# Optimization experiments

Hardware: AMD Instinct MI355X
Metric: run time of the kernel (lower is better)

Reference implementation:

```python
import jax, jax.numpy as jnp
import numpy as np

BASE = 7.0  # ModularPhaseNorm modulus


def _plane_rotate(x, theta):
    # Rotate the first 2*P dims of x in P independent 2D planes by learned angles theta [P].
    P = theta.shape[0]
    c, s = jnp.cos(theta), jnp.sin(theta)  # [P]
    head = x[..., : 2 * P].reshape(x.shape[:-1] + (P, 2))
    a, b = head[..., 0], head[..., 1]
    rot = jnp.stack([c * a - s * b, s * a + c * b], axis=-1)
    rot = rot.reshape(x.shape[:-1] + (2 * P,))
    return jnp.concatenate([rot, x[..., 2 * P :]], axis=-1)


def _modular_phase_norm(x, gamma, beta, base=BASE):
    # Wrap activations into [-base/2, base/2) (modular phase), then affine per-channel.
    wrapped = x - base * jnp.floor(x / base + 0.5)
    return gamma * wrapped + beta


def setup_inputs() -> dict:
    key = jax.random.key(0)
    ks = jax.random.split(key, 8)
    B, F, T, H = 8192, 4096, 9, 32
    team_paths = jax.random.normal(ks[0], (B, F, T), dtype=jnp.float32)
    W1 = jax.random.normal(ks[1], (F, H), dtype=jnp.float32) / np.sqrt(F)
    b1 = jnp.zeros((H,), dtype=jnp.float32)
    theta1 = jax.random.normal(ks[2], (2,), dtype=jnp.float32)  # num_rotation_planes=2
    gamma = jnp.ones((H,), dtype=jnp.float32)
    beta = jnp.zeros((H,), dtype=jnp.float32)
    W2 = jax.random.normal(ks[3], (H, 1), dtype=jnp.float32) / np.sqrt(H)
    b2 = jnp.zeros((1,), dtype=jnp.float32)
    theta2 = jax.random.normal(ks[4], (2,), dtype=jnp.float32)
    return {"team_paths": team_paths, "theta1": theta1, "W1": W1, "b1": b1,
            "gamma": gamma, "beta": beta, "theta2": theta2, "W2": W2, "b2": b2}


def reference(team_paths, theta1, W1, b1, gamma, beta, theta2, W2, b2):
    # Batch the per-member Python loop: [B, F, T] -> [B, T, F]
    x = jnp.transpose(team_paths, (0, 2, 1))
    # eidosTransform(feature_dim -> 32, 2 rotation planes)
    h = _plane_rotate(x, theta1)
    h = jnp.einsum("btf,fh->bth", h, W1) + b1
    # ModularPhaseNorm(32, base=7)
    h = _modular_phase_norm(h, gamma, beta)
    # eidosTransform(32 -> 1, 2 rotation planes)
    h = _plane_rotate(h, theta2)
    scores = jnp.einsum("bth,ho->bto", h, W2)[..., 0] + b2[0]  # [B, T]
    return jax.nn.softmax(scores, axis=1)
```

## Files before the change

### kernel.cpp

```cpp
#include <hip/hip_runtime.h>
#include <math.h>

typedef float f2v __attribute__((ext_vector_type(2)));
typedef float f4v __attribute__((ext_vector_type(4)));

#define NTILE 16
#define TILE_F 2304
#define BUF_F  4608
#define FT 36864

#define GL16(gp, lp) \
    __builtin_amdgcn_global_load_lds((const __attribute__((address_space(1))) void*)(gp), \
                                     (__attribute__((address_space(3))) void*)(lp), 16, 0, 0)
#define GL4(gp, lp) \
    __builtin_amdgcn_global_load_lds((const __attribute__((address_space(1))) void*)(gp), \
                                     (__attribute__((address_space(3))) void*)(lp), 4, 0, 0)

__global__ __launch_bounds__(256) void scorer_kernel(
    const float* __restrict__ x,
    const float* __restrict__ th1,
    const float* __restrict__ W1,
    const float* __restrict__ b1,
    const float* __restrict__ gamma,
    const float* __restrict__ beta,
    const float* __restrict__ th2,
    const float* __restrict__ W2,
    const float* __restrict__ b2p,
    float* __restrict__ out)
{
    __shared__ __align__(16) float xl[2 * BUF_F];
    const int tid = threadIdx.x;
    const int wv  = tid >> 6;
    const int hg  = tid & 7;
    const int fc  = tid >> 3;
    const int b0  = blockIdx.x * 2;
    const float* xb = x + (size_t)b0 * FT;

    f2v acc[2][9][2];
    #pragma unroll
    for (int b = 0; b < 2; ++b)
        #pragma unroll
        for (int t = 0; t < 9; ++t) {
            acc[b][t][0] = (f2v){0.f, 0.f};
            acc[b][t][1] = (f2v){0.f, 0.f};
        }

    #define STAGE(tileidx, lbuf)                                            \
        do {                                                                \
            const float* gt0 = xb + (size_t)(tileidx) * TILE_F;             \
            const float* gt1 = gt0 + FT;                                    \
            float* lb = (lbuf);                                             \
            GL16(gt0 + tid * 4,        lb + wv * 256);                      \
            GL16(gt0 + 1024 + tid * 4, lb + 1024 + wv * 256);               \
            GL4 (gt0 + 2048 + tid,     lb + 2048 + wv * 64);                \
            GL16(gt1 + tid * 4,        lb + TILE_F + wv * 256);             \
            GL16(gt1 + 1024 + tid * 4, lb + TILE_F + 1024 + wv * 256);      \
            GL4 (gt1 + 2048 + tid,     lb + TILE_F + 2048 + wv * 64);       \
        } while (0)

    STAGE(0, xl);

    int cur = 0;
    for (int tile = 0; tile < NTILE; ++tile) {
        __syncthreads();
        if (tile + 1 < NTILE)
            STAGE(tile + 1, &xl[(cur ^ 1) * BUF_F]);
        if (tile == 0) {
            if (tid < 36) {
                int bb = tid / 18, r = tid % 18, t = r >> 1, p = r & 1;
                float c = cosf(th1[p]), sn = sinf(th1[p]);
                float a  = xl[bb * TILE_F + (2 * p) * 9 + t];
                float bv = xl[bb * TILE_F + (2 * p + 1) * 9 + t];
                xl[bb * TILE_F + (2 * p) * 9 + t]     = c * a - sn * bv;
                xl[bb * TILE_F + (2 * p + 1) * 9 + t] = sn * a + c * bv;
            }
            __syncthreads();
        }
        const float* xbuf = &xl[cur * BUF_F];
        const size_t fb = (size_t)tile * 256;
        #pragma unroll
        for (int i = 0; i < 8; ++i) {
            const int row = i * 32 + fc;
            f4v wq = ((const f4v*)W1)[(fb + row) * 8 + hg];
            f2v wlo = {wq.x, wq.y}, whi = {wq.z, wq.w};
            const float* xp0 = &xbuf[row * 9];
            const float* xp1 = xp0 + TILE_F;
            #pragma unroll
            for (int t = 0; t < 9; ++t) {
                f2v x0 = {xp0[t], xp0[t]};
                f2v x1 = {xp1[t], xp1[t]};
                acc[0][t][0] += x0 * wlo;
                acc[0][t][1] += x0 * whi;
                acc[1][t][0] += x1 * wlo;
                acc[1][t][1] += x1 * whi;
            }
        }
        cur ^= 1;
    }

    const int lane = tid & 63;
    float* red = xl;
    float* redbase = &red[(wv * 8 + lane) * 72];
    #pragma unroll
    for (int b = 0; b < 2; ++b)
        #pragma unroll
        for (int t = 0; t < 9; ++t)
            #pragma unroll
            for (int jv = 0; jv < 2; ++jv) {
                f2v v = acc[b][t][jv];
                v.x += __shfl_xor(v.x, 8);  v.y += __shfl_xor(v.y, 8);
                v.x += __shfl_xor(v.x, 16); v.y += __shfl_xor(v.y, 16);
                v.x += __shfl_xor(v.x, 32); v.y += __shfl_xor(v.y, 32);
                if (lane < 8) {
                    int idx = b * 36 + t * 4 + jv * 2;
                    redbase[idx]     = v.x;
                    redbase[idx + 1] = v.y;
                }
            }
    __syncthreads();

    for (int o = tid; o < 576; o += 256) {
        int h = o & 31;
        int t = (o >> 5) % 9;
        int bb = o / 288;
        int hg2 = h >> 2, j = h & 3;
        int idx = bb * 36 + t * 4 + j;
        float v = red[(0 * 8 + hg2) * 72 + idx]
                + red[(1 * 8 + hg2) * 72 + idx]
                + red[(2 * 8 + hg2) * 72 + idx]
                + red[(3 * 8 + hg2) * 72 + idx];
        v += b1[h];
        float wr = v - 7.0f * floorf(v / 7.0f + 0.5f);
        xl[2304 + bb * 288 + t * 32 + h] = gamma[h] * wr + beta[h];
    }
    __syncthreads();

    if (tid < 18) {
        int bb = tid / 9, t = tid % 9;
        const float* g = &xl[2304 + bb * 288 + t * 32];
        float c0 = cosf(th2[0]), s0 = sinf(th2[0]);
        float c1 = cosf(th2[1]), s1 = sinf(th2[1]);
        float sc = (c0 * g[0] - s0 * g[1]) * W2[0]
                 + (s0 * g[0] + c0 * g[1]) * W2[1]
                 + (c1 * g[2] - s1 * g[3]) * W2[2]
                 + (s1 * g[2] + c1 * g[3]) * W2[3];
        #pragma unroll
        for (int h = 4; h < 32; ++h) sc += g[h] * W2[h];
        sc += b2p[0];
        xl[2880 + bb * 9 + t] = sc;
    }
    __syncthreads();

    if (tid < 18) {
        int bb = tid / 9, t = tid % 9;
        const float* sb = &xl[2880 + bb * 9];
        float m = sb[0];
        #pragma unroll
        for (int k = 1; k < 9; ++k) m = fmaxf(m, sb[k]);
        float den = 0.f;
        #pragma unroll
        for (int k = 0; k < 9; ++k) den += expf(sb[k] - m);
        out[(size_t)(b0 + bb) * 9 + t] = expf(sb[t] - m) / den;
    }
}

extern "C" void kernel_launch(void* const* d_in, const int* in_sizes, int n_in,
                              void* d_out, int out_size, void* d_ws, size_t ws_size,
                              hipStream_t stream) {
    const float* x     = (const float*)d_in[0];
    const float* th1   = (const float*)d_in[1];
    const float* W1    = (const float*)d_in[2];
    const float* b1    = (const float*)d_in[3];
    const float* gamma = (const float*)d_in[4];
    const float* beta  = (const float*)d_in[5];
    const float* th2   = (const float*)d_in[6];
    const float* W2    = (const float*)d_in[7];
    const float* b2    = (const float*)d_in[8];
    float* out = (float*)d_out;

    const int B = in_sizes[0] / FT;
    dim3 grid(B / 2), block(256);
    hipLaunchKernelGGL(scorer_kernel, grid, block, 0, stream,
                       x, th1, W1, b1, gamma, beta, th2, W2, b2, out);
}
```

Before: 439.9 us.

## Process one batch row per block with register-staged transposed LDS tiles

Each block now handles a single batch element instead of two, which doubles the grid. Tiles are prefetched with nontemporal global loads into registers and scattered into LDS in a transposed [t][f] layout, replacing the direct global-to-LDS async copies. The transposed layout lets the inner loop read x with vectorized LDS loads, and W1 rows are reassigned so each thread owns 8 consecutive features. The cost is that the W1 reuse across two batch rows is lost, so W1 traffic doubles. The scattered LDS stores may also cause bank conflicts.

```diff
diff --git a/kernel.cpp b/kernel.cpp
--- a/kernel.cpp
+++ b/kernel.cpp
@@ -5,16 +5,8 @@
 typedef float f4v __attribute__((ext_vector_type(4)));
 
 #define NTILE 16
-#define TILE_F 2304
-#define BUF_F  4608
+#define TILE_W 2304
 #define FT 36864
-
-#define GL16(gp, lp) \
-    __builtin_amdgcn_global_load_lds((const __attribute__((address_space(1))) void*)(gp), \
-                                     (__attribute__((address_space(3))) void*)(lp), 16, 0, 0)
-#define GL4(gp, lp) \
-    __builtin_amdgcn_global_load_lds((const __attribute__((address_space(1))) void*)(gp), \
-                                     (__attribute__((address_space(3))) void*)(lp), 4, 0, 0)
 
 __global__ __launch_bounds__(256) void scorer_kernel(
     const float* __restrict__ x,
@@ -28,116 +20,122 @@
     const float* __restrict__ b2p,
     float* __restrict__ out)
 {
-    __shared__ __align__(16) float xl[2 * BUF_F];
+    __shared__ __align__(16) float xl[2 * TILE_W];
     const int tid = threadIdx.x;
-    const int wv  = tid >> 6;
     const int hg  = tid & 7;
     const int fc  = tid >> 3;
-    const int b0  = blockIdx.x * 2;
-    const float* xb = x + (size_t)b0 * FT;
+    const int wv  = tid >> 6;
+    const float* xb = x + (size_t)blockIdx.x * FT;
 
-    f2v acc[2][9][2];
+    f2v acc[9][2];
     #pragma unroll
-    for (int b = 0; b < 2; ++b)
-        #pragma unroll
-        for (int t = 0; t < 9; ++t) {
-            acc[b][t][0] = (f2v){0.f, 0.f};
-            acc[b][t][1] = (f2v){0.f, 0.f};
-        }
+    for (int t = 0; t < 9; ++t) {
+        acc[t][0] = (f2v){0.f, 0.f};
+        acc[t][1] = (f2v){0.f, 0.f};
+    }
 
-    #define STAGE(tileidx, lbuf)                                            \
-        do {                                                                \
-            const float* gt0 = xb + (size_t)(tileidx) * TILE_F;             \
-            const float* gt1 = gt0 + FT;                                    \
-            float* lb = (lbuf);                                             \
-            GL16(gt0 + tid * 4,        lb + wv * 256);                      \
-            GL16(gt0 + 1024 + tid * 4, lb + 1024 + wv * 256);               \
-            GL4 (gt0 + 2048 + tid,     lb + 2048 + wv * 64);                \
-            GL16(gt1 + tid * 4,        lb + TILE_F + wv * 256);             \
-            GL16(gt1 + 1024 + tid * 4, lb + TILE_F + 1024 + wv * 256);      \
-            GL4 (gt1 + 2048 + tid,     lb + TILE_F + 2048 + wv * 64);       \
-        } while (0)
+    int laddr[9];
+    #pragma unroll
+    for (int j = 0; j < 9; ++j) {
+        int w = (j < 4) ? tid * 4 + j
+              : (j < 8) ? 1024 + tid * 4 + (j - 4)
+                        : 2048 + tid;
+        int f = (unsigned)w / 9u;
+        int t = w - 9 * f;
+        laddr[j] = t * 256 + f;
+    }
 
-    STAGE(0, xl);
+    f4v s04 = __builtin_nontemporal_load((const f4v*)(xb + tid * 4));
+    f4v s47 = __builtin_nontemporal_load((const f4v*)(xb + 1024 + tid * 4));
+    float s8 = __builtin_nontemporal_load(xb + 2048 + tid);
 
+    const f4v* __restrict__ W1v = (const f4v*)W1;
     int cur = 0;
     for (int tile = 0; tile < NTILE; ++tile) {
         __syncthreads();
-        if (tile + 1 < NTILE)
-            STAGE(tile + 1, &xl[(cur ^ 1) * BUF_F]);
+        float* lb = &xl[cur * TILE_W];
+        lb[laddr[0]] = s04.x; lb[laddr[1]] = s04.y;
+        lb[laddr[2]] = s04.z; lb[laddr[3]] = s04.w;
+        lb[laddr[4]] = s47.x; lb[laddr[5]] = s47.y;
+        lb[laddr[6]] = s47.z; lb[laddr[7]] = s47.w;
+        lb[laddr[8]] = s8;
+        __syncthreads();
+        if (tile + 1 < NTILE) {
+            const float* gt = xb + (size_t)(tile + 1) * TILE_W;
+            s04 = __builtin_nontemporal_load((const f4v*)(gt + tid * 4));
+            s47 = __builtin_nontemporal_load((const f4v*)(gt + 1024 + tid * 4));
+            s8  = __builtin_nontemporal_load(gt + 2048 + tid);
+        }
         if (tile == 0) {
-            if (tid < 36) {
-                int bb = tid / 18, r = tid % 18, t = r >> 1, p = r & 1;
+            if (tid < 18) {
+                int p = tid / 9, t = tid - p * 9;
                 float c = cosf(th1[p]), sn = sinf(th1[p]);
-                float a  = xl[bb * TILE_F + (2 * p) * 9 + t];
-                float bv = xl[bb * TILE_F + (2 * p + 1) * 9 + t];
-                xl[bb * TILE_F + (2 * p) * 9 + t]     = c * a - sn * bv;
-                xl[bb * TILE_F + (2 * p + 1) * 9 + t] = sn * a + c * bv;
+                float a  = xl[t * 256 + 2 * p];
+                float bv = xl[t * 256 + 2 * p + 1];
+                xl[t * 256 + 2 * p]     = c * a - sn * bv;
+                xl[t * 256 + 2 * p + 1] = sn * a + c * bv;
             }
             __syncthreads();
         }
-        const float* xbuf = &xl[cur * BUF_F];
-        const size_t fb = (size_t)tile * 256;
+        const int fb = tile * 256;
+        f2v wlo[8], whi[8];
         #pragma unroll
         for (int i = 0; i < 8; ++i) {
-            const int row = i * 32 + fc;
-            f4v wq = ((const f4v*)W1)[(fb + row) * 8 + hg];
-            f2v wlo = {wq.x, wq.y}, whi = {wq.z, wq.w};
-            const float* xp0 = &xbuf[row * 9];
-            const float* xp1 = xp0 + TILE_F;
-            #pragma unroll
-            for (int t = 0; t < 9; ++t) {
-                f2v x0 = {xp0[t], xp0[t]};
-                f2v x1 = {xp1[t], xp1[t]};
-                acc[0][t][0] += x0 * wlo;
-                acc[0][t][1] += x0 * whi;
-                acc[1][t][0] += x1 * wlo;
-                acc[1][t][1] += x1 * whi;
-            }
+            f4v wq = W1v[(size_t)(fb + fc * 8 + i) * 8 + hg];
+            wlo[i] = (f2v){wq.x, wq.y};
+            whi[i] = (f2v){wq.z, wq.w};
+        }
+        const float* xr = &xl[cur * TILE_W + fc * 8];
+        #pragma unroll
+        for (int t = 0; t < 9; ++t) {
+            f4v xa = *(const f4v*)(xr + t * 256);
+            f4v xc = *(const f4v*)(xr + t * 256 + 4);
+            acc[t][0] += (f2v){xa.x, xa.x} * wlo[0]; acc[t][1] += (f2v){xa.x, xa.x} * whi[0];
+            acc[t][0] += (f2v){xa.y, xa.y} * wlo[1]; acc[t][1] += (f2v){xa.y, xa.y} * whi[1];
+            acc[t][0] += (f2v){xa.z, xa.z} * wlo[2]; acc[t][1] += (f2v){xa.z, xa.z} * whi[2];
+            acc[t][0] += (f2v){xa.w, xa.w} * wlo[3]; acc[t][1] += (f2v){xa.w, xa.w} * whi[3];
+            acc[t][0] += (f2v){xc.x, xc.x} * wlo[4]; acc[t][1] += (f2v){xc.x, xc.x} * whi[4];
+            acc[t][0] += (f2v){xc.y, xc.y} * wlo[5]; acc[t][1] += (f2v){xc.y, xc.y} * whi[5];
+            acc[t][0] += (f2v){xc.z, xc.z} * wlo[6]; acc[t][1] += (f2v){xc.z, xc.z} * whi[6];
+            acc[t][0] += (f2v){xc.w, xc.w} * wlo[7]; acc[t][1] += (f2v){xc.w, xc.w} * whi[7];
         }
         cur ^= 1;
     }
 
     const int lane = tid & 63;
     float* red = xl;
-    float* redbase = &red[(wv * 8 + lane) * 72];
+    float* redbase = &red[(wv * 8 + lane) * 36];
     #pragma unroll
-    for (int b = 0; b < 2; ++b)
+    for (int t = 0; t < 9; ++t)
         #pragma unroll
-        for (int t = 0; t < 9; ++t)
-            #pragma unroll
-            for (int jv = 0; jv < 2; ++jv) {
-                f2v v = acc[b][t][jv];
-                v.x += __shfl_xor(v.x, 8);  v.y += __shfl_xor(v.y, 8);
-                v.x += __shfl_xor(v.x, 16); v.y += __shfl_xor(v.y, 16);
-                v.x += __shfl_xor(v.x, 32); v.y += __shfl_xor(v.y, 32);
-                if (lane < 8) {
-                    int idx = b * 36 + t * 4 + jv * 2;
-                    redbase[idx]     = v.x;
-                    redbase[idx + 1] = v.y;
-                }
+        for (int jv = 0; jv < 2; ++jv) {
+            f2v v = acc[t][jv];
+            v.x += __shfl_xor(v.x, 8);  v.y += __shfl_xor(v.y, 8);
+            v.x += __shfl_xor(v.x, 16); v.y += __shfl_xor(v.y, 16);
+            v.x += __shfl_xor(v.x, 32); v.y += __shfl_xor(v.y, 32);
+            if (lane < 8) {
+                redbase[t * 4 + jv * 2]     = v.x;
+                redbase[t * 4 + jv * 2 + 1] = v.y;
             }
+        }
     __syncthreads();
 
-    for (int o = tid; o < 576; o += 256) {
-        int h = o & 31;
-        int t = (o >> 5) % 9;
-        int bb = o / 288;
+    for (int o = tid; o < 288; o += 256) {
+        int h = o & 31, t = o >> 5;
         int hg2 = h >> 2, j = h & 3;
-        int idx = bb * 36 + t * 4 + j;
-        float v = red[(0 * 8 + hg2) * 72 + idx]
-                + red[(1 * 8 + hg2) * 72 + idx]
-                + red[(2 * 8 + hg2) * 72 + idx]
-                + red[(3 * 8 + hg2) * 72 + idx];
+        int idx = t * 4 + j;
+        float v = red[(0 * 8 + hg2) * 36 + idx]
+                + red[(1 * 8 + hg2) * 36 + idx]
+                + red[(2 * 8 + hg2) * 36 + idx]
+                + red[(3 * 8 + hg2) * 36 + idx];
         v += b1[h];
         float wr = v - 7.0f * floorf(v / 7.0f + 0.5f);
-        xl[2304 + bb * 288 + t * 32 + h] = gamma[h] * wr + beta[h];
+        xl[1200 + o] = gamma[h] * wr + beta[h];
     }
     __syncthreads();
 
-    if (tid < 18) {
-        int bb = tid / 9, t = tid % 9;
-        const float* g = &xl[2304 + bb * 288 + t * 32];
+    if (tid < 9) {
+        const float* g = &xl[1200 + tid * 32];
         float c0 = cosf(th2[0]), s0 = sinf(th2[0]);
         float c1 = cosf(th2[1]), s1 = sinf(th2[1]);
         float sc = (c0 * g[0] - s0 * g[1]) * W2[0]
@@ -147,20 +145,19 @@
         #pragma unroll
         for (int h = 4; h < 32; ++h) sc += g[h] * W2[h];
         sc += b2p[0];
-        xl[2880 + bb * 9 + t] = sc;
+        xl[1500 + tid] = sc;
     }
     __syncthreads();
 
-    if (tid < 18) {
-        int bb = tid / 9, t = tid % 9;
-        const float* sb = &xl[2880 + bb * 9];
+    if (tid < 9) {
+        const float* sb = &xl[1500];
         float m = sb[0];
         #pragma unroll
         for (int k = 1; k < 9; ++k) m = fmaxf(m, sb[k]);
         float den = 0.f;
         #pragma unroll
         for (int k = 0; k < 9; ++k) den += expf(sb[k] - m);
-        out[(size_t)(b0 + bb) * 9 + t] = expf(sb[t] - m) / den;
+        out[(size_t)blockIdx.x * 9 + tid] = expf(sb[tid] - m) / den;
     }
 }
 
@@ -179,7 +176,7 @@
     float* out = (float*)d_out;
 
     const int B = in_sizes[0] / FT;
-    dim3 grid(B / 2), block(256);
+    dim3 grid(B), block(256);
     hipLaunchKernelGGL(scorer_kernel, grid, block, 0, stream,
                        x, th1, W1, b1, gamma, beta, th2, W2, b2, out);
 }
```

Result: faster. 426.0 us (-3.2%).
